# Performance work log

Measured on AMD Instinct MI355X. Metric: run time of the kernel, lower is better.

Reference implementation:

```python
import jax, jax.numpy as jnp
import numpy as np

B, NQ, NK, DQ, DK, H, DV = 4, 128, 1024, 256, 256, 256, 256
MASK_VAL = -1e6


def setup_inputs() -> dict:
    key = jax.random.key(0)
    ks = jax.random.split(key, 7)
    queries = jax.random.normal(ks[0], (B, NQ, DQ), dtype=jnp.float32)
    keys = jax.random.normal(ks[1], (B, NK, DK), dtype=jnp.float32)
    values = jax.random.normal(ks[2], (B, NK, DV), dtype=jnp.float32)
    # per-batch valid lengths in [1, NK]
    valid_lens = jax.random.randint(ks[3], (B,), 1, NK + 1, dtype=jnp.int64 if jax.config.read('jax_enable_x64') else jnp.int32)
    W_q = jax.random.normal(ks[4], (DQ, H), dtype=jnp.float32) * (1.0 / np.sqrt(DQ))
    W_k = jax.random.normal(ks[5], (DK, H), dtype=jnp.float32) * (1.0 / np.sqrt(DK))
    v_w = jax.random.normal(ks[6], (H,), dtype=jnp.float32) * (1.0 / np.sqrt(H))
    return {"queries": queries, "keys": keys, "values": values,
            "valid_lens": valid_lens, "W_q": W_q, "W_k": W_k, "v_w": v_w}


def reference(queries, keys, values, valid_lens, W_q, W_k, v_w):
    # Project queries and keys to the shared hidden space.
    q = jnp.einsum('bqd,dh->bqh', queries, W_q)          # (B, NQ, H)
    k = jnp.einsum('bkd,dh->bkh', keys, W_k)             # (B, NK, H)
    # Broadcast-add + tanh -> (B, NQ, NK, H), then contract with v to scores.
    features = jnp.tanh(q[:, :, None, :] + k[:, None, :, :])
    scores = jnp.einsum('bqkh,h->bqk', features, v_w)    # (B, NQ, NK)
    # Masked softmax over the key axis: positions >= valid_len get -1e6.
    nk = scores.shape[-1]
    mask = jnp.arange(nk)[None, None, :] < valid_lens[:, None, None]
    scores = jnp.where(mask, scores, MASK_VAL)
    attention_weights = jax.nn.softmax(scores, axis=-1)
    # Weighted sum of values (bmm).
    return jnp.einsum('bqk,bkv->bqv', attention_weights, values)
```

## Files before the change

kernel.cpp:

```cpp
#include <hip/hip_runtime.h>

#define B_   4
#define NQ_  128
#define NK_  1024
#define DD_  256
#define H_   256
#define DV_  256

__device__ __forceinline__ float wave_sum(float v) {
  #pragma unroll
  for (int o = 32; o; o >>= 1) v += __shfl_xor(v, o);
  return v;
}
__device__ __forceinline__ float wave_max(float v) {
  #pragma unroll
  for (int o = 32; o; o >>= 1) v = fmaxf(v, __shfl_xor(v, o));
  return v;
}

__global__ __launch_bounds__(256) void proj_merged_kernel(
    const float* __restrict__ queries, const float* __restrict__ keys,
    const float* __restrict__ W_q, const float* __restrict__ W_k,
    float* __restrict__ qp, float* __restrict__ kpT) {
  __shared__ float As[16 * 68];
  __shared__ float Ws[16 * 68];
  __shared__ float Ts[64 * 68];
  const int tid  = threadIdx.x;
  const int row0 = blockIdx.x * 64;
  const int col0 = blockIdx.y * 64;
  const bool isQ = row0 < 512;
  const float* A = isQ ? queries + (size_t)row0 * DD_
                       : keys + (size_t)(row0 - 512) * DD_;
  const float* W = isQ ? W_q : W_k;
  const int ld_d = tid & 15, ld_r = tid >> 4;
  const int lw_n = tid & 63, lw_k = tid >> 6;
  const int tn = tid & 15, tm = tid >> 4;

  float aP[4], wP[4];
  #pragma unroll
  for (int p = 0; p < 4; ++p) aP[p] = A[(size_t)(p * 16 + ld_r) * DD_ + ld_d];
  #pragma unroll
  for (int p = 0; p < 4; ++p) wP[p] = W[(size_t)(p * 4 + lw_k) * H_ + col0 + lw_n];

  float acc[4][4] = {};
  for (int kt = 0; kt < 16; ++kt) {
    __syncthreads();
    #pragma unroll
    for (int p = 0; p < 4; ++p) As[ld_d * 68 + p * 16 + ld_r] = aP[p];
    #pragma unroll
    for (int p = 0; p < 4; ++p) Ws[(p * 4 + lw_k) * 68 + lw_n] = wP[p];
    __syncthreads();
    if (kt < 15) {
      const int k0 = (kt + 1) * 16;
      #pragma unroll
      for (int p = 0; p < 4; ++p) aP[p] = A[(size_t)(p * 16 + ld_r) * DD_ + k0 + ld_d];
      #pragma unroll
      for (int p = 0; p < 4; ++p) wP[p] = W[(size_t)(k0 + p * 4 + lw_k) * H_ + col0 + lw_n];
    }
    #pragma unroll
    for (int kk = 0; kk < 16; ++kk) {
      const float4 a = *(const float4*)&As[kk * 68 + tm * 4];
      const float4 w = *(const float4*)&Ws[kk * 68 + tn * 4];
      acc[0][0] = fmaf(a.x, w.x, acc[0][0]);
      acc[0][1] = fmaf(a.x, w.y, acc[0][1]);
      acc[0][2] = fmaf(a.x, w.z, acc[0][2]);
      acc[0][3] = fmaf(a.x, w.w, acc[0][3]);
      acc[1][0] = fmaf(a.y, w.x, acc[1][0]);
      acc[1][1] = fmaf(a.y, w.y, acc[1][1]);
      acc[1][2] = fmaf(a.y, w.z, acc[1][2]);
      acc[1][3] = fmaf(a.y, w.w, acc[1][3]);
      acc[2][0] = fmaf(a.z, w.x, acc[2][0]);
      acc[2][1] = fmaf(a.z, w.y, acc[2][1]);
      acc[2][2] = fmaf(a.z, w.z, acc[2][2]);
      acc[2][3] = fmaf(a.z, w.w, acc[2][3]);
      acc[3][0] = fmaf(a.w, w.x, acc[3][0]);
      acc[3][1] = fmaf(a.w, w.y, acc[3][1]);
      acc[3][2] = fmaf(a.w, w.z, acc[3][2]);
      acc[3][3] = fmaf(a.w, w.w, acc[3][3]);
    }
  }

  if (isQ) {
    #pragma unroll
    for (int i = 0; i < 4; ++i) {
      *(float4*)&qp[(size_t)(row0 + tm * 4 + i) * H_ + col0 + tn * 4] =
          make_float4(acc[i][0], acc[i][1], acc[i][2], acc[i][3]);
    }
  } else {
    #pragma unroll
    for (int i = 0; i < 4; ++i)
      #pragma unroll
      for (int j = 0; j < 4; ++j)
        Ts[(tn * 4 + j) * 68 + tm * 4 + i] = acc[i][j];
    __syncthreads();
    const int keyrow = row0 - 512;
    const int b = keyrow >> 10;
    const int kbase = keyrow & (NK_ - 1);
    const int hh = tid >> 2;
    const int kg = (tid & 3) * 16;
    float* dst = kpT + ((size_t)(b * H_ + col0 + hh)) * NK_ + kbase + kg;
    #pragma unroll
    for (int p = 0; p < 4; ++p)
      *(float4*)&dst[p * 4] = *(const float4*)&Ts[hh * 68 + kg + p * 4];
  }
}

__global__ __launch_bounds__(512) void fused_attn_kernel(
    const float* __restrict__ qp, const float* __restrict__ kpT,
    const float* __restrict__ v_w, const float* __restrict__ values,
    const int* __restrict__ valid_lens, float* __restrict__ out) {
  __shared__ float2 qs2[H_];
  __shared__ float w2s[H_];
  __shared__ float reds[4];
  __shared__ float s_half[2][2][NK_];
  __shared__ float redm[2][4];
  __shared__ float redsum[2][4];
  __shared__ float red[8][2][DV_];

  const int tid = threadIdx.x;
  const int n = blockIdx.x;
  const int xcd = n & 7;
  const int b = xcd >> 1;
  const int idx = ((n >> 3) << 1) | (xcd & 1);
  const int qrow = b * NQ_ + idx * 2;

  int vl = valid_lens[b];
  vl = vl < 1 ? 1 : (vl > NK_ ? NK_ : vl);

  const float C2 = 2.8853900817779268f;
  if (tid < H_) {
    const float vw = v_w[tid];
    w2s[tid] = 2.0f * vw;
    const float q0 = qp[(size_t)qrow * H_ + tid];
    const float q1 = qp[(size_t)(qrow + 1) * H_ + tid];
    qs2[tid] = make_float2(q0 * C2, q1 * C2);
    float s = wave_sum(vw);
    if ((tid & 63) == 0) reds[tid >> 6] = s;
  }
  __syncthreads();
  const float wsum = reds[0] + reds[1] + reds[2] + reds[3];

  const int g = tid >> 8;
  const int t = tid & 255;
  const int k0 = t * 4;
  if (k0 < vl) {
    float a0x = 0.f, a0y = 0.f, a0z = 0.f, a0w = 0.f;
    float a1x = 0.f, a1y = 0.f, a1z = 0.f, a1w = 0.f;
    const float* kp = kpT + (size_t)b * H_ * NK_ + (size_t)(g * 128) * NK_ + k0;
    #pragma unroll 2
    for (int h = 0; h < 128; ++h) {
      const float4 kv = *(const float4*)(kp + (size_t)h * NK_);
      const int hh = g * 128 + h;
      const float w2 = w2s[hh];
      const float2 q2 = qs2[hh];
      const float e0x = __builtin_amdgcn_exp2f(fmaf(kv.x, C2, q2.x));
      const float e0y = __builtin_amdgcn_exp2f(fmaf(kv.y, C2, q2.x));
      const float e0z = __builtin_amdgcn_exp2f(fmaf(kv.z, C2, q2.x));
      const float e0w = __builtin_amdgcn_exp2f(fmaf(kv.w, C2, q2.x));
      const float e1x = __builtin_amdgcn_exp2f(fmaf(kv.x, C2, q2.y));
      const float e1y = __builtin_amdgcn_exp2f(fmaf(kv.y, C2, q2.y));
      const float e1z = __builtin_amdgcn_exp2f(fmaf(kv.z, C2, q2.y));
      const float e1w = __builtin_amdgcn_exp2f(fmaf(kv.w, C2, q2.y));
      a0x = fmaf(w2, __builtin_amdgcn_rcpf(1.0f + e0x), a0x);
      a0y = fmaf(w2, __builtin_amdgcn_rcpf(1.0f + e0y), a0y);
      a0z = fmaf(w2, __builtin_amdgcn_rcpf(1.0f + e0z), a0z);
      a0w = fmaf(w2, __builtin_amdgcn_rcpf(1.0f + e0w), a0w);
      a1x = fmaf(w2, __builtin_amdgcn_rcpf(1.0f + e1x), a1x);
      a1y = fmaf(w2, __builtin_amdgcn_rcpf(1.0f + e1y), a1y);
      a1z = fmaf(w2, __builtin_amdgcn_rcpf(1.0f + e1z), a1z);
      a1w = fmaf(w2, __builtin_amdgcn_rcpf(1.0f + e1w), a1w);
    }
    *(float4*)&s_half[g][0][k0] = make_float4(a0x, a0y, a0z, a0w);
    *(float4*)&s_half[g][1][k0] = make_float4(a1x, a1y, a1z, a1w);
  }
  __syncthreads();

  const int qi = tid >> 8;
  const int k4 = (tid & 255) * 4;
  const float4 pA = *(const float4*)&s_half[0][qi][k4];
  const float4 pB = *(const float4*)&s_half[1][qi][k4];
  const float s0 = wsum - (pA.x + pB.x);
  const float s1 = wsum - (pA.y + pB.y);
  const float s2 = wsum - (pA.z + pB.z);
  const float s3 = wsum - (pA.w + pB.w);
  const float NEG = -3.0e38f;
  float m = NEG;
  m = fmaxf(m, (k4 + 0 < vl) ? s0 : NEG);
  m = fmaxf(m, (k4 + 1 < vl) ? s1 : NEG);
  m = fmaxf(m, (k4 + 2 < vl) ? s2 : NEG);
  m = fmaxf(m, (k4 + 3 < vl) ? s3 : NEG);
  m = wave_max(m);
  if ((tid & 63) == 0) redm[qi][(tid >> 6) & 3] = m;
  __syncthreads();
  const float M = fmaxf(fmaxf(redm[qi][0], redm[qi][1]),
                        fmaxf(redm[qi][2], redm[qi][3]));
  const float CE = 1.4426950408889634f;
  const float p0 = (k4 + 0 < vl) ? __builtin_amdgcn_exp2f((s0 - M) * CE) : 0.0f;
  const float p1 = (k4 + 1 < vl) ? __builtin_amdgcn_exp2f((s1 - M) * CE) : 0.0f;
  const float p2 = (k4 + 2 < vl) ? __builtin_amdgcn_exp2f((s2 - M) * CE) : 0.0f;
  const float p3 = (k4 + 3 < vl) ? __builtin_amdgcn_exp2f((s3 - M) * CE) : 0.0f;
  float psum = wave_sum(p0 + p1 + p2 + p3);
  if ((tid & 63) == 0) redsum[qi][(tid >> 6) & 3] = psum;
  __syncthreads();
  const float S = redsum[qi][0] + redsum[qi][1] + redsum[qi][2] + redsum[qi][3];
  const float inv = 1.0f / S;
  *(float4*)&s_half[0][qi][k4] = make_float4(p0 * inv, p1 * inv, p2 * inv, p3 * inv);
  __syncthreads();

  const int w = tid >> 6;
  const int lane = tid & 63;
  const int d0 = lane * 4;
  float4 pa0 = make_float4(0.f, 0.f, 0.f, 0.f);
  float4 pa1 = make_float4(0.f, 0.f, 0.f, 0.f);
  const int kbeg = w * (NK_ / 8);
  const int kend = (kbeg + NK_ / 8) < vl ? (kbeg + NK_ / 8) : vl;
  const float* vb = values + (size_t)b * NK_ * DV_ + d0;
  #pragma unroll 4
  for (int k = kbeg; k < kend; ++k) {
    const float4 v4 = *(const float4*)(vb + (size_t)k * DV_);
    const float w0 = s_half[0][0][k];
    const float w1 = s_half[0][1][k];
    pa0.x = fmaf(w0, v4.x, pa0.x);
    pa0.y = fmaf(w0, v4.y, pa0.y);
    pa0.z = fmaf(w0, v4.z, pa0.z);
    pa0.w = fmaf(w0, v4.w, pa0.w);
    pa1.x = fmaf(w1, v4.x, pa1.x);
    pa1.y = fmaf(w1, v4.y, pa1.y);
    pa1.z = fmaf(w1, v4.z, pa1.z);
    pa1.w = fmaf(w1, v4.w, pa1.w);
  }
  *(float4*)&red[w][0][d0] = pa0;
  *(float4*)&red[w][1][d0] = pa1;
  __syncthreads();

  const int oqi = tid >> 8;
  const int d = tid & 255;
  float s = 0.f;
  #pragma unroll
  for (int ww = 0; ww < 8; ++ww) s += red[ww][oqi][d];
  out[(size_t)(qrow + oqi) * DV_ + d] = s;
}

extern "C" void kernel_launch(void* const* d_in, const int* in_sizes, int n_in,
                              void* d_out, int out_size, void* d_ws, size_t ws_size,
                              hipStream_t stream) {
  const float* queries = (const float*)d_in[0];
  const float* keys    = (const float*)d_in[1];
  const float* values  = (const float*)d_in[2];
  const int*   vlens   = (const int*)d_in[3];
  const float* W_q     = (const float*)d_in[4];
  const float* W_k     = (const float*)d_in[5];
  const float* v_w     = (const float*)d_in[6];
  float* out = (float*)d_out;

  float* qp  = (float*)d_ws;
  float* kpT = qp + (size_t)B_ * NQ_ * H_;

  proj_merged_kernel<<<dim3((512 + B_ * NK_) / 64, H_ / 64), 256, 0, stream>>>(
      queries, keys, W_q, W_k, qp, kpT);
  fused_attn_kernel<<<(B_ * NQ_) / 2, 512, 0, stream>>>(qp, kpT, v_w, values, vlens, out);
}
```

Baseline: 132.1 us.

## Shrink projection row tile and add register prefetch in score and PV loops

```diff
diff --git a/kernel.cpp b/kernel.cpp
--- a/kernel.cpp
+++ b/kernel.cpp
@@ -22,11 +22,11 @@
     const float* __restrict__ queries, const float* __restrict__ keys,
     const float* __restrict__ W_q, const float* __restrict__ W_k,
     float* __restrict__ qp, float* __restrict__ kpT) {
-  __shared__ float As[16 * 68];
+  __shared__ float As[16 * 36];
   __shared__ float Ws[16 * 68];
-  __shared__ float Ts[64 * 68];
+  __shared__ float Ts[64 * 36];
   const int tid  = threadIdx.x;
-  const int row0 = blockIdx.x * 64;
+  const int row0 = blockIdx.x * 32;
   const int col0 = blockIdx.y * 64;
   const bool isQ = row0 < 512;
   const float* A = isQ ? queries + (size_t)row0 * DD_
@@ -36,30 +36,30 @@
   const int lw_n = tid & 63, lw_k = tid >> 6;
   const int tn = tid & 15, tm = tid >> 4;
 
-  float aP[4], wP[4];
-  #pragma unroll
-  for (int p = 0; p < 4; ++p) aP[p] = A[(size_t)(p * 16 + ld_r) * DD_ + ld_d];
+  float aP[2], wP[4];
+  #pragma unroll
+  for (int p = 0; p < 2; ++p) aP[p] = A[(size_t)(p * 16 + ld_r) * DD_ + ld_d];
   #pragma unroll
   for (int p = 0; p < 4; ++p) wP[p] = W[(size_t)(p * 4 + lw_k) * H_ + col0 + lw_n];
 
-  float acc[4][4] = {};
+  float acc[2][4] = {};
   for (int kt = 0; kt < 16; ++kt) {
     __syncthreads();
     #pragma unroll
-    for (int p = 0; p < 4; ++p) As[ld_d * 68 + p * 16 + ld_r] = aP[p];
+    for (int p = 0; p < 2; ++p) As[ld_d * 36 + p * 16 + ld_r] = aP[p];
     #pragma unroll
     for (int p = 0; p < 4; ++p) Ws[(p * 4 + lw_k) * 68 + lw_n] = wP[p];
     __syncthreads();
     if (kt < 15) {
       const int k0 = (kt + 1) * 16;
       #pragma unroll
-      for (int p = 0; p < 4; ++p) aP[p] = A[(size_t)(p * 16 + ld_r) * DD_ + k0 + ld_d];
+      for (int p = 0; p < 2; ++p) aP[p] = A[(size_t)(p * 16 + ld_r) * DD_ + k0 + ld_d];
       #pragma unroll
       for (int p = 0; p < 4; ++p) wP[p] = W[(size_t)(k0 + p * 4 + lw_k) * H_ + col0 + lw_n];
     }
     #pragma unroll
     for (int kk = 0; kk < 16; ++kk) {
-      const float4 a = *(const float4*)&As[kk * 68 + tm * 4];
+      const float2 a = *(const float2*)&As[kk * 36 + tm * 2];
       const float4 w = *(const float4*)&Ws[kk * 68 + tn * 4];
       acc[0][0] = fmaf(a.x, w.x, acc[0][0]);
       acc[0][1] = fmaf(a.x, w.y, acc[0][1]);
@@ -69,39 +69,31 @@
       acc[1][1] = fmaf(a.y, w.y, acc[1][1]);
       acc[1][2] = fmaf(a.y, w.z, acc[1][2]);
       acc[1][3] = fmaf(a.y, w.w, acc[1][3]);
-      acc[2][0] = fmaf(a.z, w.x, acc[2][0]);
-      acc[2][1] = fmaf(a.z, w.y, acc[2][1]);
-      acc[2][2] = fmaf(a.z, w.z, acc[2][2]);
-      acc[2][3] = fmaf(a.z, w.w, acc[2][3]);
-      acc[3][0] = fmaf(a.w, w.x, acc[3][0]);
-      acc[3][1] = fmaf(a.w, w.y, acc[3][1]);
-      acc[3][2] = fmaf(a.w, w.z, acc[3][2]);
-      acc[3][3] = fmaf(a.w, w.w, acc[3][3]);
     }
   }
 
   if (isQ) {
     #pragma unroll
-    for (int i = 0; i < 4; ++i) {
-      *(float4*)&qp[(size_t)(row0 + tm * 4 + i) * H_ + col0 + tn * 4] =
+    for (int i = 0; i < 2; ++i) {
+      *(float4*)&qp[(size_t)(row0 + tm * 2 + i) * H_ + col0 + tn * 4] =
           make_float4(acc[i][0], acc[i][1], acc[i][2], acc[i][3]);
     }
   } else {
     #pragma unroll
-    for (int i = 0; i < 4; ++i)
+    for (int i = 0; i < 2; ++i)
       #pragma unroll
       for (int j = 0; j < 4; ++j)
-        Ts[(tn * 4 + j) * 68 + tm * 4 + i] = acc[i][j];
+        Ts[(tn * 4 + j) * 36 + tm * 2 + i] = acc[i][j];
     __syncthreads();
     const int keyrow = row0 - 512;
     const int b = keyrow >> 10;
     const int kbase = keyrow & (NK_ - 1);
     const int hh = tid >> 2;
-    const int kg = (tid & 3) * 16;
+    const int kg = (tid & 3) * 8;
     float* dst = kpT + ((size_t)(b * H_ + col0 + hh)) * NK_ + kbase + kg;
     #pragma unroll
-    for (int p = 0; p < 4; ++p)
-      *(float4*)&dst[p * 4] = *(const float4*)&Ts[hh * 68 + kg + p * 4];
+    for (int p = 0; p < 2; ++p)
+      *(float4*)&dst[p * 4] = *(const float4*)&Ts[hh * 36 + kg + p * 4];
   }
 }
 
@@ -141,35 +133,55 @@
   const float wsum = reds[0] + reds[1] + reds[2] + reds[3];
 
   const int g = tid >> 8;
-  const int t = tid & 255;
-  const int k0 = t * 4;
+  const int k0 = (tid & 255) * 4;
   if (k0 < vl) {
     float a0x = 0.f, a0y = 0.f, a0z = 0.f, a0w = 0.f;
     float a1x = 0.f, a1y = 0.f, a1z = 0.f, a1w = 0.f;
-    const float* kp = kpT + (size_t)b * H_ * NK_ + (size_t)(g * 128) * NK_ + k0;
-    #pragma unroll 2
-    for (int h = 0; h < 128; ++h) {
-      const float4 kv = *(const float4*)(kp + (size_t)h * NK_);
-      const int hh = g * 128 + h;
-      const float w2 = w2s[hh];
-      const float2 q2 = qs2[hh];
-      const float e0x = __builtin_amdgcn_exp2f(fmaf(kv.x, C2, q2.x));
-      const float e0y = __builtin_amdgcn_exp2f(fmaf(kv.y, C2, q2.x));
-      const float e0z = __builtin_amdgcn_exp2f(fmaf(kv.z, C2, q2.x));
-      const float e0w = __builtin_amdgcn_exp2f(fmaf(kv.w, C2, q2.x));
-      const float e1x = __builtin_amdgcn_exp2f(fmaf(kv.x, C2, q2.y));
-      const float e1y = __builtin_amdgcn_exp2f(fmaf(kv.y, C2, q2.y));
-      const float e1z = __builtin_amdgcn_exp2f(fmaf(kv.z, C2, q2.y));
-      const float e1w = __builtin_amdgcn_exp2f(fmaf(kv.w, C2, q2.y));
-      a0x = fmaf(w2, __builtin_amdgcn_rcpf(1.0f + e0x), a0x);
-      a0y = fmaf(w2, __builtin_amdgcn_rcpf(1.0f + e0y), a0y);
-      a0z = fmaf(w2, __builtin_amdgcn_rcpf(1.0f + e0z), a0z);
-      a0w = fmaf(w2, __builtin_amdgcn_rcpf(1.0f + e0w), a0w);
-      a1x = fmaf(w2, __builtin_amdgcn_rcpf(1.0f + e1x), a1x);
-      a1y = fmaf(w2, __builtin_amdgcn_rcpf(1.0f + e1y), a1y);
-      a1z = fmaf(w2, __builtin_amdgcn_rcpf(1.0f + e1z), a1z);
-      a1w = fmaf(w2, __builtin_amdgcn_rcpf(1.0f + e1w), a1w);
-    }
+    const float* kp = kpT + ((size_t)(b * H_ + g * 128)) * NK_ + k0;
+    const float* w2p = w2s + g * 128;
+    const float2* q2p = qs2 + g * 128;
+    float4 c0 = *(const float4*)(kp + 0 * (size_t)NK_);
+    float4 c1 = *(const float4*)(kp + 1 * (size_t)NK_);
+    float4 c2 = *(const float4*)(kp + 2 * (size_t)NK_);
+    float4 c3 = *(const float4*)(kp + 3 * (size_t)NK_);
+#define CONSUME(kv, h)                                                     \
+    {                                                                      \
+      const float w2 = w2p[h];                                             \
+      const float2 q2 = q2p[h];                                            \
+      const float e0x = __builtin_amdgcn_exp2f(fmaf((kv).x, C2, q2.x));    \
+      const float e0y = __builtin_amdgcn_exp2f(fmaf((kv).y, C2, q2.x));    \
+      const float e0z = __builtin_amdgcn_exp2f(fmaf((kv).z, C2, q2.x));    \
+      const float e0w = __builtin_amdgcn_exp2f(fmaf((kv).w, C2, q2.x));    \
+      const float e1x = __builtin_amdgcn_exp2f(fmaf((kv).x, C2, q2.y));    \
+      const float e1y = __builtin_amdgcn_exp2f(fmaf((kv).y, C2, q2.y));    \
+      const float e1z = __builtin_amdgcn_exp2f(fmaf((kv).z, C2, q2.y));    \
+      const float e1w = __builtin_amdgcn_exp2f(fmaf((kv).w, C2, q2.y));    \
+      a0x = fmaf(w2, __builtin_amdgcn_rcpf(1.0f + e0x), a0x);              \
+      a0y = fmaf(w2, __builtin_amdgcn_rcpf(1.0f + e0y), a0y);              \
+      a0z = fmaf(w2, __builtin_amdgcn_rcpf(1.0f + e0z), a0z);              \
+      a0w = fmaf(w2, __builtin_amdgcn_rcpf(1.0f + e0w), a0w);              \
+      a1x = fmaf(w2, __builtin_amdgcn_rcpf(1.0f + e1x), a1x);              \
+      a1y = fmaf(w2, __builtin_amdgcn_rcpf(1.0f + e1y), a1y);              \
+      a1z = fmaf(w2, __builtin_amdgcn_rcpf(1.0f + e1z), a1z);              \
+      a1w = fmaf(w2, __builtin_amdgcn_rcpf(1.0f + e1w), a1w);              \
+    }
+    for (int gg = 0; gg < 31; ++gg) {
+      const int hb = gg * 4;
+      const float4 n0 = *(const float4*)(kp + (size_t)(hb + 4) * NK_);
+      const float4 n1 = *(const float4*)(kp + (size_t)(hb + 5) * NK_);
+      const float4 n2 = *(const float4*)(kp + (size_t)(hb + 6) * NK_);
+      const float4 n3 = *(const float4*)(kp + (size_t)(hb + 7) * NK_);
+      CONSUME(c0, hb + 0)
+      CONSUME(c1, hb + 1)
+      CONSUME(c2, hb + 2)
+      CONSUME(c3, hb + 3)
+      c0 = n0; c1 = n1; c2 = n2; c3 = n3;
+    }
+    CONSUME(c0, 124)
+    CONSUME(c1, 125)
+    CONSUME(c2, 126)
+    CONSUME(c3, 127)
+#undef CONSUME
     *(float4*)&s_half[g][0][k0] = make_float4(a0x, a0y, a0z, a0w);
     *(float4*)&s_half[g][1][k0] = make_float4(a1x, a1y, a1z, a1w);
   }
@@ -215,20 +227,47 @@
   const int kbeg = w * (NK_ / 8);
   const int kend = (kbeg + NK_ / 8) < vl ? (kbeg + NK_ / 8) : vl;
   const float* vb = values + (size_t)b * NK_ * DV_ + d0;
-  #pragma unroll 4
-  for (int k = kbeg; k < kend; ++k) {
+#define PVSTEP(v4, kk)                                                     \
+    {                                                                      \
+      const float w0 = s_half[0][0][kk];                                   \
+      const float w1 = s_half[0][1][kk];                                   \
+      pa0.x = fmaf(w0, (v4).x, pa0.x);                                     \
+      pa0.y = fmaf(w0, (v4).y, pa0.y);                                     \
+      pa0.z = fmaf(w0, (v4).z, pa0.z);                                     \
+      pa0.w = fmaf(w0, (v4).w, pa0.w);                                     \
+      pa1.x = fmaf(w1, (v4).x, pa1.x);                                     \
+      pa1.y = fmaf(w1, (v4).y, pa1.y);                                     \
+      pa1.z = fmaf(w1, (v4).z, pa1.z);                                     \
+      pa1.w = fmaf(w1, (v4).w, pa1.w);                                     \
+    }
+  int k = kbeg;
+  if (k + 4 <= kend) {
+    float4 v0 = *(const float4*)(vb + (size_t)(k + 0) * DV_);
+    float4 v1 = *(const float4*)(vb + (size_t)(k + 1) * DV_);
+    float4 v2 = *(const float4*)(vb + (size_t)(k + 2) * DV_);
+    float4 v3 = *(const float4*)(vb + (size_t)(k + 3) * DV_);
+    for (; k + 8 <= kend; k += 4) {
+      const float4 u0 = *(const float4*)(vb + (size_t)(k + 4) * DV_);
+      const float4 u1 = *(const float4*)(vb + (size_t)(k + 5) * DV_);
+      const float4 u2 = *(const float4*)(vb + (size_t)(k + 6) * DV_);
+      const float4 u3 = *(const float4*)(vb + (size_t)(k + 7) * DV_);
+      PVSTEP(v0, k + 0)
+      PVSTEP(v1, k + 1)
+      PVSTEP(v2, k + 2)
+      PVSTEP(v3, k + 3)
+      v0 = u0; v1 = u1; v2 = u2; v3 = u3;
+    }
+    PVSTEP(v0, k + 0)
+    PVSTEP(v1, k + 1)
+    PVSTEP(v2, k + 2)
+    PVSTEP(v3, k + 3)
+    k += 4;
+  }
+  for (; k < kend; ++k) {
     const float4 v4 = *(const float4*)(vb + (size_t)k * DV_);
-    const float w0 = s_half[0][0][k];
-    const float w1 = s_half[0][1][k];
-    pa0.x = fmaf(w0, v4.x, pa0.x);
-    pa0.y = fmaf(w0, v4.y, pa0.y);
-    pa0.z = fmaf(w0, v4.z, pa0.z);
-    pa0.w = fmaf(w0, v4.w, pa0.w);
-    pa1.x = fmaf(w1, v4.x, pa1.x);
-    pa1.y = fmaf(w1, v4.y, pa1.y);
-    pa1.z = fmaf(w1, v4.z, pa1.z);
-    pa1.w = fmaf(w1, v4.w, pa1.w);
-  }
+    PVSTEP(v4, k)
+  }
+#undef PVSTEP
   *(float4*)&red[w][0][d0] = pa0;
   *(float4*)&red[w][1][d0] = pa1;
   __syncthreads();
@@ -256,7 +295,7 @@
   float* qp  = (float*)d_ws;
   float* kpT = qp + (size_t)B_ * NQ_ * H_;
 
-  proj_merged_kernel<<<dim3((512 + B_ * NK_) / 64, H_ / 64), 256, 0, stream>>>(
+  proj_merged_kernel<<<dim3((512 + B_ * NK_) / 32, H_ / 64), 256, 0, stream>>>(
       queries, keys, W_q, W_k, qp, kpT);
   fused_attn_kernel<<<(B_ * NQ_) / 2, 512, 0, stream>>>(qp, kpT, v_w, values, vlens, out);
 }
```

Result: faster. 123.5 us (-6.5%).
